# Performance work log

Hardware: AMD Instinct MI355X
Metric: run time of the kernel (lower is better)

The kernel has to match this reference:

```python
import jax, jax.numpy as jnp
import numpy as np
from jax import lax

SCORE_T = 0.05
NMS_T = 0.5
MAXDET = 300


def batch_iou(b1, b2):
    # b1: [K,4], b2: [K,4] -> [K,K]
    lt = jnp.maximum(b1[:, None, :2], b2[None, :, :2])
    rb = jnp.minimum(b1[:, None, 2:], b2[None, :, 2:])
    inter = jnp.clip(rb - lt, 0.0, None).prod(-1)
    a1 = (b1[:, 2:] - b1[:, :2]).prod(-1)
    a2 = (b2[:, 2:] - b2[:, :2]).prod(-1)
    union = a1[:, None] + a2[None, :] - inter
    return inter / jnp.clip(union, 1e-7, None)


def nms_class(boxes, cls_scores):
    # boxes: [N,4], cls_scores: [N]. Mirrors: score>thresh filter, top-k MAXDET
    # candidates, greedy NMS in descending score order.
    s = jnp.where(cls_scores > SCORE_T, cls_scores, -jnp.inf)
    top_s, idx = lax.top_k(s, MAXDET)          # sorted desc, [K]
    b = jnp.take(boxes, idx, axis=0)            # [K,4]
    v = jnp.isfinite(top_s)                     # passed score threshold
    iou = batch_iou(b, b)                       # [K,K]

    def body(kept, i):
        # keep i iff valid and no already-kept box has IoU >= NMS_T with it
        suppressed = jnp.any(jnp.where(kept, iou[i], 0.0) >= NMS_T)
        return kept.at[i].set(v[i] & ~suppressed), None

    kept, _ = lax.scan(body, jnp.zeros(MAXDET, dtype=bool), jnp.arange(MAXDET))
    return top_s, idx, kept


def per_image(boxes, cls):
    # boxes: [N,4], cls: [N,C]
    C = cls.shape[1]
    top_s, idx, kept = jax.vmap(nms_class, in_axes=(None, 1))(boxes, cls)  # [C,K]
    scores_flat = jnp.where(kept, top_s, -jnp.inf).reshape(-1)  # [C*K]
    idx_flat = idx.reshape(-1)
    labels_flat = jnp.repeat(jnp.arange(C), MAXDET)
    fs, fi = lax.top_k(scores_flat, MAXDET)     # global top-k across classes
    valid = jnp.isfinite(fs)
    box_idx = idx_flat[fi]
    out_boxes = jnp.where(valid[:, None], jnp.take(boxes, box_idx, axis=0), -1.0)
    out_scores = jnp.where(valid, fs, -1.0)
    out_labels = jnp.where(valid, labels_flat[fi], -1).astype(jnp.int32)
    return out_boxes, out_scores, out_labels


def setup_inputs() -> dict:
    key = jax.random.key(0)
    k1, k2, k3 = jax.random.split(key, 3)
    B, N, C = 8, 100000, 80
    centers = jax.random.uniform(k1, (B, N, 2), dtype=jnp.float32) * 1024.0
    wh = jax.random.uniform(k2, (B, N, 2), dtype=jnp.float32) * 96.0 + 4.0
    boxes = jnp.concatenate([centers - wh / 2, centers + wh / 2], axis=-1)
    classification = jax.random.uniform(k3, (B, N, C), dtype=jnp.float32)
    return {"boxes": boxes, "classification": classification}


def reference(boxes, classification):
    # Returns (Boxes [B,MAXDET,4], Scores [B,MAXDET], Labels [B,MAXDET] int32),
    # padded with -1 where fewer than MAXDET detections survive.
    return jax.vmap(per_image)(boxes, classification)
```

## Files before the change

### kernel.cpp

```cpp
#include <hip/hip_runtime.h>

#define BIMG 8
#define NBOX 100000
#define NCLS 80
#define KDET 300
#define CAP  2048
#define CAPC 12
#define TPUSH 0.9921875f
#define SCORE_T 0.05f
#define NELEM 8000000
#define NQ    2000000

typedef unsigned long long u64;
typedef unsigned u32;

#define OFF_PUSHCNT 0u
#define ZERO_BYTES  2560u
#define OFF_BUF     4096u
#define OFF_KCNT    (4096u + 10485760u)
#define OFF_KSC     (OFF_KCNT + 2560u)
#define OFF_KIDX    (OFF_KSC + 768000u)

static __device__ __forceinline__ u64 mk_key(float sc, u32 n) {
  return ((u64)__float_as_uint(sc) << 32) | (u32)(~n);
}

static __device__ __forceinline__ u64 shr64(u64 v, int s) {
  return (s >= 64) ? 0ull : (v >> s);
}

static __device__ __forceinline__ void radix_step(const u32* hist, u32* sk,
                                                  u64* spfx, u32* ssel) {
  if (threadIdx.x < 64) {
    const int lane = threadIdx.x;
    const int chunk = 32;
    u32 psum = 0;
    for (int i = 0; i < chunk; ++i) psum += hist[lane * chunk + i];
    u32 suf = psum;
#pragma unroll
    for (int off = 1; off < 64; off <<= 1) {
      u32 o = __shfl_down(suf, off);
      if (lane + off < 64) suf += o;
    }
    u32 k = *sk;
    u64 bal = __ballot(suf >= k);
    if (bal != 0ull) {
      int L = 63 - __clzll((long long)bal);
      if (lane == L) {
        u32 krem = k - (suf - psum);
        int bi = (L + 1) * chunk - 1;
        u32 acc = 0;
        for (;;) {
          acc += hist[bi];
          if (acc >= krem || bi == L * chunk) break;
          --bi;
        }
        *spfx = (*spfx << 11) | (u32)bi;
        *sk = krem - (acc - hist[bi]);
        *ssel = (suf - psum) + acc;
      }
    }
  }
}

static __device__ __forceinline__ void pushone(int c, float sc, u32 n, int b,
                                               u32* lcnt, u64* stage,
                                               u32* pushcnt, u64* buf) {
  u64 key = mk_key(sc, n);
  u32 slot = atomicAdd(&lcnt[c], 1u);
  if (slot < CAPC) {
    stage[c * CAPC + slot] = key;
  } else {
    u32 g = atomicAdd(&pushcnt[b * NCLS + c], 1u);
    if (g < CAP) buf[(size_t)(b * NCLS + c) * CAP + g] = key;
  }
}

__global__ __launch_bounds__(256) void histK(const float* __restrict__ cls,
                                             u32* __restrict__ pushcnt,
                                             u64* __restrict__ buf) {
  __shared__ u32 lcnt[NCLS];
  __shared__ u32 sbase[NCLS];
  __shared__ u64 stage[NCLS * CAPC];

  const int t = threadIdx.x;
  const int b = blockIdx.y;
  for (int i = t; i < NCLS; i += 256) lcnt[i] = 0;
  __syncthreads();

  const float4* base4 = (const float4*)(cls + (size_t)b * NELEM);
  const int start = blockIdx.x * 8192;

#define PROCQ(u) do { \
    float mx = fmaxf(fmaxf(v##u.x, v##u.y), fmaxf(v##u.z, v##u.w)); \
    if (mx >= TPUSH) { \
      const int e0 = q##u * 4; \
      const int c0 = e0 % NCLS; \
      const u32 n = (u32)(e0 / NCLS); \
      if (v##u.x >= TPUSH) pushone(c0 + 0, v##u.x, n, b, lcnt, stage, pushcnt, buf); \
      if (v##u.y >= TPUSH) pushone(c0 + 1, v##u.y, n, b, lcnt, stage, pushcnt, buf); \
      if (v##u.z >= TPUSH) pushone(c0 + 2, v##u.z, n, b, lcnt, stage, pushcnt, buf); \
      if (v##u.w >= TPUSH) pushone(c0 + 3, v##u.w, n, b, lcnt, stage, pushcnt, buf); \
    } } while (0)

  if (start + 8192 <= NQ) {
    for (int it = 0; it < 4; ++it) {
      const int qb = start + it * 2048 + t;
#define LOADF(u) const int q##u = qb + (u) * 256; const float4 v##u = base4[q##u]
      LOADF(0); LOADF(1); LOADF(2); LOADF(3);
      LOADF(4); LOADF(5); LOADF(6); LOADF(7);
#undef LOADF
      PROCQ(0); PROCQ(1); PROCQ(2); PROCQ(3);
      PROCQ(4); PROCQ(5); PROCQ(6); PROCQ(7);
    }
  } else {
    for (int it = 0; it < 4; ++it) {
      const int qb = start + it * 2048 + t;
#define LOADC(u) const int q##u = qb + (u) * 256; \
  const float4 v##u = (q##u < NQ) ? base4[q##u] : make_float4(0.f, 0.f, 0.f, 0.f)
      LOADC(0); LOADC(1); LOADC(2); LOADC(3);
      LOADC(4); LOADC(5); LOADC(6); LOADC(7);
#undef LOADC
      PROCQ(0); PROCQ(1); PROCQ(2); PROCQ(3);
      PROCQ(4); PROCQ(5); PROCQ(6); PROCQ(7);
    }
  }
#undef PROCQ
  __syncthreads();

  if (t < NCLS) {
    u32 cnt = min(lcnt[t], (u32)CAPC);
    sbase[t] = cnt ? atomicAdd(&pushcnt[b * NCLS + t], cnt) : 0u;
  }
  __syncthreads();
  for (int idx = t; idx < NCLS * CAPC; idx += 256) {
    const int c = idx / CAPC;
    const int k = idx - c * CAPC;
    if ((u32)k < min(lcnt[c], (u32)CAPC)) {
      u32 s = sbase[c] + (u32)k;
      if (s < CAP) buf[(size_t)(b * NCLS + c) * CAP + s] = stage[idx];
    }
  }
}

__global__ __launch_bounds__(512) void nmsK(const float* __restrict__ boxes,
                                            const float* __restrict__ cls,
                                            const u32* __restrict__ pushcnt,
                                            u64* __restrict__ buf,
                                            u32* __restrict__ keptCnt,
                                            float* __restrict__ keptScore,
                                            u32* __restrict__ keptIdx) {
  __shared__ float bx[KDET][5];
  __shared__ float scl[KDET];
  __shared__ u32 nn_[KDET];
  __shared__ u64 msk[KDET][5];
  __shared__ u64 tk[512];
  __shared__ u64 keptw[5];
  __shared__ u64 spfx;
  __shared__ u64 sand, sor;
  __shared__ u32 sk, ssel, stcnt;
  __shared__ u32 sfpfx, sfk, sfab, sfeq, sfmode, sfbcnt;

  const int t = threadIdx.x;
  const int bc = blockIdx.x;
  const int b = bc / NCLS;
  u64* bufp = buf + (size_t)bc * CAP;
  u32* hist = (u32*)&msk[0][0];

  if (t == 0) { spfx = 0ull; sk = KDET; stcnt = 0u; sfmode = 0u; sfbcnt = 0u; }

  u32 realcnt = pushcnt[bc];
  const bool dofb = !(realcnt >= (u32)KDET && realcnt <= (u32)CAP);
  if (dofb) {
    const int c = bc % NCLS;
    const float* col = cls + (size_t)b * NELEM + c;
    for (int r = 0; r < 3; ++r) {
      const int shift = (r == 0) ? 21 : (r == 1) ? 10 : 0;
      const int nbins = (r == 2) ? 1024 : 2048;
      for (int i = t; i < nbins; i += 512) hist[i] = 0;
      __syncthreads();
      for (int n = t; n < NBOX; n += 512) {
        float sc = col[(size_t)n * NCLS];
        if (sc > SCORE_T) {
          u32 u = __float_as_uint(sc);
          bool ok = (r == 0) || (r == 1 ? ((u >> 21) == (sfpfx >> 21))
                                        : ((u >> 10) == (sfpfx >> 10)));
          if (ok) atomicAdd(&hist[(u >> shift) & (u32)(nbins - 1)], 1u);
        }
      }
      __syncthreads();
      if (t == 0) {
        if (r == 0) {
          u32 s = 0;
          for (int i = 0; i < nbins; ++i) s += hist[i];
          if (s < KDET) sfmode = 1u;
        }
        if (sfmode == 0u) {
          u32 kk2 = (r == 0) ? (u32)KDET : sfk;
          u32 acc = 0;
          int bi = nbins - 1;
          for (; bi >= 0; --bi) {
            if (acc + hist[bi] >= kk2) break;
            acc += hist[bi];
          }
          sfk = kk2 - acc;
          sfpfx = ((r == 0) ? 0u : sfpfx) | ((u32)bi << shift);
          if (r == 2) { sfeq = hist[bi]; sfab = KDET - sfk; }
        }
      }
      __syncthreads();
      if (sfmode == 1u) break;
    }

    if (sfmode == 1u) {
      for (int n = t; n < NBOX; n += 512) {
        float sc = col[(size_t)n * NCLS];
        if (sc > SCORE_T) {
          u32 g = atomicAdd(&sfbcnt, 1u);
          if (g < CAP) bufp[g] = mk_key(sc, (u32)n);
        }
      }
    } else {
      const u32 ustar = sfpfx;
      const u32 m = sfab, e = sfeq;
      if (m + e <= CAP) {
        for (int n = t; n < NBOX; n += 512) {
          float sc = col[(size_t)n * NCLS];
          if (sc > SCORE_T && __float_as_uint(sc) >= ustar) {
            u32 g = atomicAdd(&sfbcnt, 1u);
            if (g < CAP) bufp[g] = mk_key(sc, (u32)n);
          }
        }
      } else {
        for (int n = t; n < NBOX; n += 512) {
          float sc = col[(size_t)n * NCLS];
          if (sc > SCORE_T && __float_as_uint(sc) > ustar) {
            u32 g = atomicAdd(&sfbcnt, 1u);
            if (g < CAP) bufp[g] = mk_key(sc, (u32)n);
          }
        }
        __syncthreads();
        if (t == 0) {
          u32 room = CAP - m, got = 0;
          for (int n = 0; n < NBOX && got < room; ++n) {
            float sc = col[(size_t)n * NCLS];
            if (sc > SCORE_T && __float_as_uint(sc) == ustar) {
              u32 g = atomicAdd(&sfbcnt, 1u);
              if (g < CAP) bufp[g] = mk_key(sc, (u32)n);
              ++got;
            }
          }
        }
      }
    }
    __threadfence_block();
    __syncthreads();
    realcnt = sfbcnt;
  }
  const int cnt = min((int)realcnt, CAP);

  u64 kk[4];
#pragma unroll
  for (int u = 0; u < 4; ++u) {
    int i = t + u * 512;
    u64 v = 0ull;
    if (i < cnt)
      v = dofb ? *((volatile const u64*)(bufp + i)) : bufp[i];
    kk[u] = v;
  }

  const bool normal = (cnt > KDET);
  int eshift = 0;
  u64 ethr = 1ull;
  if (normal) {
    if (t == 0) { sand = ~0ull; sor = 0ull; }
    __syncthreads();
    {
      u64 ka = ~0ull, ko = 0ull;
#pragma unroll
      for (int u = 0; u < 4; ++u) {
        u64 key = kk[u];
        if (key) { ka &= key; ko |= key; }
      }
#pragma unroll
      for (int off = 32; off > 0; off >>= 1) {
        ka &= __shfl_xor(ka, off);
        ko |= __shfl_xor(ko, off);
      }
      if ((t & 63) == 0) {
        atomicAnd((unsigned long long*)&sand, (unsigned long long)ka);
        atomicOr((unsigned long long*)&sor, (unsigned long long)ko);
      }
    }
    __syncthreads();
    const u64 kand = sand, kor = sor;
    const u64 W = kand ^ kor;
    const int hv = 63 - __clzll((long long)W);
    int s = 11 * (hv / 11);
    if (t == 0) spfx = shr64(kand, s + 11);
    for (;;) {
      for (int i = t; i < 2048; i += 512) hist[i] = 0;
      __syncthreads();
      const u64 pfxHi = spfx;
      const u32 skPrev = sk;
#pragma unroll
      for (int u = 0; u < 4; ++u) {
        u64 key = kk[u];
        if (!key) continue;
        if (shr64(key, s + 11) != pfxHi) continue;
        atomicAdd(&hist[(u32)(key >> s) & 2047u], 1u);
      }
      __syncthreads();
      radix_step(hist, &sk, &spfx, &ssel);
      __syncthreads();
      if ((u32)KDET - skPrev + ssel <= 512u || s == 0) { eshift = s; break; }
      s -= 11;
    }
    ethr = spfx;
  } else {
    __syncthreads();
  }

  tk[t] = 0ull;
  __syncthreads();
  {
    const int lane = t & 63;
    const u64 lmlt = (1ull << lane) - 1ull;
#pragma unroll
    for (int u = 0; u < 4; ++u) {
      u64 key = kk[u];
      bool q = (key != 0ull) && (shr64(key, eshift) >= ethr);
      u64 bal = __ballot(q);
      u32 nw = (u32)__popcll(bal);
      if (nw) {
        u32 base = 0;
        if (lane == 0) base = atomicAdd(&stcnt, nw);
        base = __shfl(base, 0);
        if (q) {
          u32 pos = base + (u32)__popcll(bal & lmlt);
          if (pos < 512) tk[pos] = key;
        }
      }
    }
  }
  __syncthreads();

  const int sc = min((int)stcnt, 512);
  const int M = min(sc, KDET);
  {
    const u64 mykey = tk[t];
    const int scU = (sc + 7) & ~7;
    int rank = 0;
    for (int j = 0; j < scU; j += 8) {
#pragma unroll
      for (int jj = 0; jj < 8; ++jj) rank += (tk[j + jj] > mykey) ? 1 : 0;
    }
    if (mykey != 0ull && rank < KDET) {
      u32 n = ~(u32)mykey;
      scl[rank] = __uint_as_float((u32)(mykey >> 32));
      nn_[rank] = n;
      const float4 bv = *(const float4*)(boxes + ((size_t)b * NBOX + n) * 4);
      bx[rank][0] = bv.x; bx[rank][1] = bv.y; bx[rank][2] = bv.z; bx[rank][3] = bv.w;
    }
  }
  __syncthreads();

  for (int tau = t; tau < KDET * 5; tau += 512) {
    const int i = tau / 5;
    const int w = tau - i * 5;
    u64 m = 0ull;
    const int jb = w << 6;
    if (i < M && jb < i) {
      const int je = min(i, jb + 64);
      const float x1 = bx[i][0], y1 = bx[i][1], x2 = bx[i][2], y2 = bx[i][3];
      const float a1 = (x2 - x1) * (y2 - y1);
      for (int j = jb; j < je; ++j) {
        float lx = fmaxf(x1, bx[j][0]);
        float ly = fmaxf(y1, bx[j][1]);
        float rx = fminf(x2, bx[j][2]);
        float ry = fminf(y2, bx[j][3]);
        float iw = fmaxf(rx - lx, 0.0f), ih = fmaxf(ry - ly, 0.0f);
        float inter = iw * ih;
        float a2 = (bx[j][2] - bx[j][0]) * (bx[j][3] - bx[j][1]);
        float uni = fmaxf(a1 + a2 - inter, 1e-7f);
        float iou = inter / uni;
        if (iou >= 0.5f) m |= 1ull << (j & 63);
      }
    }
    if (i < M) msk[i][w] = m;
  }
  __syncthreads();

  if (t < 64) {
    u64 kwv[5];
#pragma unroll
    for (int w = 0; w < 5; ++w) {
      const int i = w * 64 + t;
      bool pb = (i < M);
      u64 mown = 0ull;
      if (pb) {
#pragma unroll
        for (int w2 = 0; w2 < 5; ++w2)
          if (w2 < w && (msk[i][w2] & kwv[w2])) pb = false;
        mown = msk[i][w];
      }
      u64 kv = 0ull;
      for (;;) {
        u64 bal = __ballot(pb && ((mown & kv) == 0ull));
        if (!bal) break;
        int p = __ffsll((unsigned long long)bal) - 1;
        kv |= 1ull << p;
        if (t == p) pb = false;
      }
      kwv[w] = kv;
      if (t == 0) keptw[w] = kv;
    }
  }
  __syncthreads();

  for (int i = t; i < M; i += 512) {
    if ((keptw[i >> 6] >> (i & 63)) & 1ull) {
      int rank = 0;
      for (int w = 0; w < (i >> 6); ++w) rank += __popcll(keptw[w]);
      rank += __popcll(keptw[i >> 6] & ((1ull << (i & 63)) - 1ull));
      keptScore[(size_t)bc * KDET + rank] = scl[i];
      keptIdx[(size_t)bc * KDET + rank] = nn_[i];
    }
  }
  if (t == 0) {
    int tot = 0;
    for (int w = 0; w < 5; ++w) tot += __popcll(keptw[w]);
    keptCnt[bc] = (u32)tot;
  }
}

__global__ __launch_bounds__(512) void mergeK(const float* __restrict__ boxes,
                                              const u32* __restrict__ keptCnt,
                                              const float* __restrict__ keptScore,
                                              const u32* __restrict__ keptIdx,
                                              float* __restrict__ out) {
  __shared__ u32 hist[2048];
  __shared__ int msc[NCLS];
  __shared__ u64 tk[512];
  __shared__ u64 spfx, sand, sor;
  __shared__ u32 sk, ssel, stcnt, smtot;

  const int t = threadIdx.x;
  const int b = blockIdx.x;
  if (t < NCLS) msc[t] = min((int)keptCnt[b * NCLS + t], KDET);
  if (t == 0) {
    spfx = 0ull; sk = KDET; stcnt = 0u; smtot = 0u; sand = ~0ull; sor = 0ull;
  }
  __syncthreads();

  const float* ksc = keptScore + (size_t)b * NCLS * KDET;
#define MKEY(idx, key) do { \
    int c_ = (idx) / KDET, r_ = (idx) - c_ * KDET; \
    key = (r_ < msc[c_]) ? ((u64)__float_as_uint(ksc[idx]) << 32) | (u32)(~(u32)(idx)) \
                         : 0ull; \
  } while (0)

  {
    u64 ka = ~0ull, ko = 0ull;
    u32 mycnt = 0;
    for (int idx = t; idx < NCLS * KDET; idx += 512) {
      u64 key; MKEY(idx, key);
      if (key) { ka &= key; ko |= key; ++mycnt; }
    }
#pragma unroll
    for (int off = 32; off > 0; off >>= 1) {
      ka &= __shfl_xor(ka, off);
      ko |= __shfl_xor(ko, off);
      mycnt += __shfl_xor(mycnt, off);
    }
    if ((t & 63) == 0) {
      atomicAnd((unsigned long long*)&sand, (unsigned long long)ka);
      atomicOr((unsigned long long*)&sor, (unsigned long long)ko);
      atomicAdd(&smtot, mycnt);
    }
  }
  __syncthreads();

  const bool mnormal = ((int)smtot > KDET);
  int eshift = 0;
  u64 ethr = 1ull;
  if (mnormal) {
    const u64 kand = sand, kor = sor;
    const u64 W = kand ^ kor;
    const int hv = 63 - __clzll((long long)W);
    int s = 11 * (hv / 11);
    if (t == 0) spfx = shr64(kand, s + 11);
    for (;;) {
      for (int i = t; i < 2048; i += 512) hist[i] = 0;
      __syncthreads();
      const u64 pfxHi = spfx;
      const u32 skPrev = sk;
      for (int idx = t; idx < NCLS * KDET; idx += 512) {
        u64 key; MKEY(idx, key);
        if (!key) continue;
        if (shr64(key, s + 11) != pfxHi) continue;
        atomicAdd(&hist[(u32)(key >> s) & 2047u], 1u);
      }
      __syncthreads();
      radix_step(hist, &sk, &spfx, &ssel);
      __syncthreads();
      if ((u32)KDET - skPrev + ssel <= 512u || s == 0) { eshift = s; break; }
      s -= 11;
    }
    ethr = spfx;
  }

  tk[t] = 0ull;
  __syncthreads();
  {
    const int lane = t & 63;
    const u64 lmlt = (1ull << lane) - 1ull;
    for (int i0 = 0; i0 < NCLS * KDET; i0 += 512) {
      const int idx = i0 + t;
      u64 key = 0ull;
      if (idx < NCLS * KDET) MKEY(idx, key);
      bool q = (key != 0ull) && (shr64(key, eshift) >= ethr);
      u64 bal = __ballot(q);
      u32 nw = (u32)__popcll(bal);
      if (nw) {
        u32 base = 0;
        if (lane == 0) base = atomicAdd(&stcnt, nw);
        base = __shfl(base, 0);
        if (q) {
          u32 pos = base + (u32)__popcll(bal & lmlt);
          if (pos < 512) tk[pos] = key;
        }
      }
    }
  }
  __syncthreads();
#undef MKEY

  const int sc = min((int)stcnt, 512);
  {
    const u64 mykey = tk[t];
    const int scU = (sc + 7) & ~7;
    int rank = 0;
    for (int j = 0; j < scU; j += 8) {
#pragma unroll
      for (int jj = 0; jj < 8; ++jj) rank += (tk[j + jj] > mykey) ? 1 : 0;
    }
    __syncthreads();
    tk[t] = 0ull;
    __syncthreads();
    if (mykey != 0ull && rank < KDET) tk[rank] = mykey;
  }
  __syncthreads();

  if (t < KDET) {
    float* ob = out + ((size_t)b * KDET + t) * 4;
    float* os = out + (size_t)BIMG * KDET * 4;
    float* ol = os + (size_t)BIMG * KDET;
    u64 key = tk[t];
    if (key == 0ull) {
      *(float4*)ob = make_float4(-1.f, -1.f, -1.f, -1.f);
      os[(size_t)b * KDET + t] = -1.f;
      ol[(size_t)b * KDET + t] = -1.f;
    } else {
      u32 fi = ~(u32)key;
      int c = fi / KDET, r = fi - c * KDET;
      u32 n = keptIdx[((size_t)b * NCLS + c) * KDET + r];
      *(float4*)ob = *(const float4*)(boxes + ((size_t)b * NBOX + n) * 4);
      os[(size_t)b * KDET + t] = __uint_as_float((u32)(key >> 32));
      ol[(size_t)b * KDET + t] = (float)c;
    }
  }
}

extern "C" void kernel_launch(void* const* d_in, const int* in_sizes, int n_in,
                              void* d_out, int out_size, void* d_ws, size_t ws_size,
                              hipStream_t stream) {
  const float* boxes = (const float*)d_in[0];
  const float* cls = (const float*)d_in[1];
  float* out = (float*)d_out;
  char* ws = (char*)d_ws;

  u32* pushcnt = (u32*)(ws + OFF_PUSHCNT);
  u64* buf = (u64*)(ws + OFF_BUF);
  u32* keptCnt = (u32*)(ws + OFF_KCNT);
  float* keptScore = (float*)(ws + OFF_KSC);
  u32* keptIdx = (u32*)(ws + OFF_KIDX);

  (void)hipMemsetAsync(ws + OFF_PUSHCNT, 0, ZERO_BYTES, stream);

  histK<<<dim3(245, BIMG), 256, 0, stream>>>(cls, pushcnt, buf);
  nmsK<<<BIMG * NCLS, 512, 0, stream>>>(boxes, cls, pushcnt, buf, keptCnt,
                                        keptScore, keptIdx);
  mergeK<<<BIMG, 512, 0, stream>>>(boxes, keptCnt, keptScore, keptIdx, out);
}
```

Baseline: 520.3 us.

## Replace per-class NMS and merge with per-image score-ordered chunked greedy NMS

The candidate push threshold is raised, and all candidates for an image go into one global buffer through a single per-image atomic counter. This replaces the per-class staged buffers. The separate per-class NMS kernel (640 blocks) and the merge kernel become one 1024-thread block per image. That block takes candidates in descending global score order in chunks of 512, runs class-aware greedy NMS against the boxes already kept, and stops once 300 are kept. A slow per-class radix-select fallback over the full score matrix runs when the buffer overflows or too few detections survive. The aim is to cut push atomics, buffer traffic and the redundant per-class work, at the cost of only 8 blocks of parallelism in the NMS stage.

```diff
diff --git a/kernel.cpp b/kernel.cpp
--- a/kernel.cpp
+++ b/kernel.cpp
@@ -4,9 +4,10 @@
 #define NBOX 100000
 #define NCLS 80
 #define KDET 300
-#define CAP  2048
-#define CAPC 12
-#define TPUSH 0.9921875f
+#define CAP2 8192
+#define PCCAP 2048
+#define BUFSTRIDE (NCLS * PCCAP)
+#define TPUSH2 0.999755859375f
 #define SCORE_T 0.05f
 #define NELEM 8000000
 #define NQ    2000000
@@ -14,19 +15,15 @@
 typedef unsigned long long u64;
 typedef unsigned u32;
 
-#define OFF_PUSHCNT 0u
-#define ZERO_BYTES  2560u
-#define OFF_BUF     4096u
-#define OFF_KCNT    (4096u + 10485760u)
-#define OFF_KSC     (OFF_KCNT + 2560u)
-#define OFF_KIDX    (OFF_KSC + 768000u)
-
-static __device__ __forceinline__ u64 mk_key(float sc, u32 n) {
-  return ((u64)__float_as_uint(sc) << 32) | (u32)(~n);
-}
+#define OFF_PCNT 0u
+#define ZERO_BYTES 32u
+#define OFF_BUF  4096u
 
 static __device__ __forceinline__ u64 shr64(u64 v, int s) {
   return (s >= 64) ? 0ull : (v >> s);
+}
+static __device__ __forceinline__ u64 key2(float sc, u32 c, u32 n) {
+  return ((u64)__float_as_uint(sc) << 32) | (u32)(~(c * (u32)NBOX + n));
 }
 
 static __device__ __forceinline__ void radix_step(const u32* hist, u32* sk,
@@ -63,44 +60,28 @@
   }
 }
 
-static __device__ __forceinline__ void pushone(int c, float sc, u32 n, int b,
-                                               u32* lcnt, u64* stage,
-                                               u32* pushcnt, u64* buf) {
-  u64 key = mk_key(sc, n);
-  u32 slot = atomicAdd(&lcnt[c], 1u);
-  if (slot < CAPC) {
-    stage[c * CAPC + slot] = key;
-  } else {
-    u32 g = atomicAdd(&pushcnt[b * NCLS + c], 1u);
-    if (g < CAP) buf[(size_t)(b * NCLS + c) * CAP + g] = key;
-  }
-}
-
 __global__ __launch_bounds__(256) void histK(const float* __restrict__ cls,
-                                             u32* __restrict__ pushcnt,
+                                             u32* __restrict__ pcnt,
                                              u64* __restrict__ buf) {
-  __shared__ u32 lcnt[NCLS];
-  __shared__ u32 sbase[NCLS];
-  __shared__ u64 stage[NCLS * CAPC];
-
   const int t = threadIdx.x;
   const int b = blockIdx.y;
-  for (int i = t; i < NCLS; i += 256) lcnt[i] = 0;
-  __syncthreads();
-
   const float4* base4 = (const float4*)(cls + (size_t)b * NELEM);
+  u64* bufb = buf + (size_t)b * BUFSTRIDE;
   const int start = blockIdx.x * 8192;
 
+#define PUSH1(cc, sc_) do { \
+    u32 g = atomicAdd(&pcnt[b], 1u); \
+    if (g < CAP2) bufb[g] = key2(sc_, (u32)(cc), (u32)n); } while (0)
 #define PROCQ(u) do { \
     float mx = fmaxf(fmaxf(v##u.x, v##u.y), fmaxf(v##u.z, v##u.w)); \
-    if (mx >= TPUSH) { \
+    if (mx >= TPUSH2) { \
       const int e0 = q##u * 4; \
       const int c0 = e0 % NCLS; \
-      const u32 n = (u32)(e0 / NCLS); \
-      if (v##u.x >= TPUSH) pushone(c0 + 0, v##u.x, n, b, lcnt, stage, pushcnt, buf); \
-      if (v##u.y >= TPUSH) pushone(c0 + 1, v##u.y, n, b, lcnt, stage, pushcnt, buf); \
-      if (v##u.z >= TPUSH) pushone(c0 + 2, v##u.z, n, b, lcnt, stage, pushcnt, buf); \
-      if (v##u.w >= TPUSH) pushone(c0 + 3, v##u.w, n, b, lcnt, stage, pushcnt, buf); \
+      const int n = e0 / NCLS; \
+      if (v##u.x >= TPUSH2) PUSH1(c0 + 0, v##u.x); \
+      if (v##u.y >= TPUSH2) PUSH1(c0 + 1, v##u.y); \
+      if (v##u.z >= TPUSH2) PUSH1(c0 + 2, v##u.z); \
+      if (v##u.w >= TPUSH2) PUSH1(c0 + 3, v##u.w); \
     } } while (0)
 
   if (start + 8192 <= NQ) {
@@ -126,448 +107,371 @@
     }
   }
 #undef PROCQ
-  __syncthreads();
-
-  if (t < NCLS) {
-    u32 cnt = min(lcnt[t], (u32)CAPC);
-    sbase[t] = cnt ? atomicAdd(&pushcnt[b * NCLS + t], cnt) : 0u;
-  }
-  __syncthreads();
-  for (int idx = t; idx < NCLS * CAPC; idx += 256) {
-    const int c = idx / CAPC;
-    const int k = idx - c * CAPC;
-    if ((u32)k < min(lcnt[c], (u32)CAPC)) {
-      u32 s = sbase[c] + (u32)k;
-      if (s < CAP) buf[(size_t)(b * NCLS + c) * CAP + s] = stage[idx];
-    }
-  }
-}
-
-__global__ __launch_bounds__(512) void nmsK(const float* __restrict__ boxes,
-                                            const float* __restrict__ cls,
-                                            const u32* __restrict__ pushcnt,
-                                            u64* __restrict__ buf,
-                                            u32* __restrict__ keptCnt,
-                                            float* __restrict__ keptScore,
-                                            u32* __restrict__ keptIdx) {
-  __shared__ float bx[KDET][5];
-  __shared__ float scl[KDET];
-  __shared__ u32 nn_[KDET];
-  __shared__ u64 msk[KDET][5];
-  __shared__ u64 tk[512];
-  __shared__ u64 keptw[5];
-  __shared__ u64 spfx;
-  __shared__ u64 sand, sor;
-  __shared__ u32 sk, ssel, stcnt;
-  __shared__ u32 sfpfx, sfk, sfab, sfeq, sfmode, sfbcnt;
-
-  const int t = threadIdx.x;
-  const int bc = blockIdx.x;
-  const int b = bc / NCLS;
-  u64* bufp = buf + (size_t)bc * CAP;
+#undef PUSH1
+}
+
+__global__ __launch_bounds__(1024) void nmsK(const float* __restrict__ boxes,
+                                             const float* __restrict__ cls,
+                                             const u32* __restrict__ pcnt,
+                                             u64* __restrict__ buf,
+                                             float* __restrict__ out) {
+  __shared__ u64 msk[512][8];
+  __shared__ u64 ks[512];
+  __shared__ float bx[512][5];
+  __shared__ u32 ci[512];
+  __shared__ u32 valid[512];
+  __shared__ u64 kkey[KDET];
+  __shared__ float kbx[KDET][4];
+  __shared__ u32 ccnt[NCLS], chunkcls[NCLS];
+  __shared__ u64 keptw[8];
+  __shared__ u64 sand, sor, spfx, swin;
+  __shared__ u32 sk, ssel, stcnt, srem, skcnt, scap;
+  __shared__ u32 srtot, sfpfx, sfk, sfab, sfeq, sfmode, slocal;
+
   u32* hist = (u32*)&msk[0][0];
-
-  if (t == 0) { spfx = 0ull; sk = KDET; stcnt = 0u; sfmode = 0u; sfbcnt = 0u; }
-
-  u32 realcnt = pushcnt[bc];
-  const bool dofb = !(realcnt >= (u32)KDET && realcnt <= (u32)CAP);
-  if (dofb) {
-    const int c = bc % NCLS;
-    const float* col = cls + (size_t)b * NELEM + c;
-    for (int r = 0; r < 3; ++r) {
-      const int shift = (r == 0) ? 21 : (r == 1) ? 10 : 0;
-      const int nbins = (r == 2) ? 1024 : 2048;
-      for (int i = t; i < nbins; i += 512) hist[i] = 0;
-      __syncthreads();
-      for (int n = t; n < NBOX; n += 512) {
-        float sc = col[(size_t)n * NCLS];
-        if (sc > SCORE_T) {
-          u32 u = __float_as_uint(sc);
-          bool ok = (r == 0) || (r == 1 ? ((u >> 21) == (sfpfx >> 21))
-                                        : ((u >> 10) == (sfpfx >> 10)));
-          if (ok) atomicAdd(&hist[(u >> shift) & (u32)(nbins - 1)], 1u);
-        }
-      }
-      __syncthreads();
-      if (t == 0) {
-        if (r == 0) {
-          u32 s = 0;
-          for (int i = 0; i < nbins; ++i) s += hist[i];
-          if (s < KDET) sfmode = 1u;
-        }
-        if (sfmode == 0u) {
-          u32 kk2 = (r == 0) ? (u32)KDET : sfk;
-          u32 acc = 0;
-          int bi = nbins - 1;
-          for (; bi >= 0; --bi) {
-            if (acc + hist[bi] >= kk2) break;
-            acc += hist[bi];
-          }
-          sfk = kk2 - acc;
-          sfpfx = ((r == 0) ? 0u : sfpfx) | ((u32)bi << shift);
-          if (r == 2) { sfeq = hist[bi]; sfab = KDET - sfk; }
-        }
-      }
-      __syncthreads();
-      if (sfmode == 1u) break;
-    }
-
-    if (sfmode == 1u) {
-      for (int n = t; n < NBOX; n += 512) {
-        float sc = col[(size_t)n * NCLS];
-        if (sc > SCORE_T) {
-          u32 g = atomicAdd(&sfbcnt, 1u);
-          if (g < CAP) bufp[g] = mk_key(sc, (u32)n);
-        }
-      }
-    } else {
-      const u32 ustar = sfpfx;
-      const u32 m = sfab, e = sfeq;
-      if (m + e <= CAP) {
-        for (int n = t; n < NBOX; n += 512) {
-          float sc = col[(size_t)n * NCLS];
-          if (sc > SCORE_T && __float_as_uint(sc) >= ustar) {
-            u32 g = atomicAdd(&sfbcnt, 1u);
-            if (g < CAP) bufp[g] = mk_key(sc, (u32)n);
-          }
-        }
-      } else {
-        for (int n = t; n < NBOX; n += 512) {
-          float sc = col[(size_t)n * NCLS];
-          if (sc > SCORE_T && __float_as_uint(sc) > ustar) {
-            u32 g = atomicAdd(&sfbcnt, 1u);
-            if (g < CAP) bufp[g] = mk_key(sc, (u32)n);
-          }
-        }
-        __syncthreads();
-        if (t == 0) {
-          u32 room = CAP - m, got = 0;
-          for (int n = 0; n < NBOX && got < room; ++n) {
-            float sc = col[(size_t)n * NCLS];
-            if (sc > SCORE_T && __float_as_uint(sc) == ustar) {
-              u32 g = atomicAdd(&sfbcnt, 1u);
-              if (g < CAP) bufp[g] = mk_key(sc, (u32)n);
-              ++got;
-            }
-          }
-        }
-      }
-    }
-    __threadfence_block();
-    __syncthreads();
-    realcnt = sfbcnt;
-  }
-  const int cnt = min((int)realcnt, CAP);
-
-  u64 kk[4];
-#pragma unroll
-  for (int u = 0; u < 4; ++u) {
-    int i = t + u * 512;
-    u64 v = 0ull;
-    if (i < cnt)
-      v = dofb ? *((volatile const u64*)(bufp + i)) : bufp[i];
-    kk[u] = v;
-  }
-
-  const bool normal = (cnt > KDET);
-  int eshift = 0;
-  u64 ethr = 1ull;
-  if (normal) {
-    if (t == 0) { sand = ~0ull; sor = 0ull; }
-    __syncthreads();
-    {
-      u64 ka = ~0ull, ko = 0ull;
-#pragma unroll
-      for (int u = 0; u < 4; ++u) {
-        u64 key = kk[u];
-        if (key) { ka &= key; ko |= key; }
-      }
-#pragma unroll
-      for (int off = 32; off > 0; off >>= 1) {
-        ka &= __shfl_xor(ka, off);
-        ko |= __shfl_xor(ko, off);
-      }
-      if ((t & 63) == 0) {
-        atomicAnd((unsigned long long*)&sand, (unsigned long long)ka);
-        atomicOr((unsigned long long*)&sor, (unsigned long long)ko);
-      }
-    }
-    __syncthreads();
-    const u64 kand = sand, kor = sor;
-    const u64 W = kand ^ kor;
-    const int hv = 63 - __clzll((long long)W);
-    int s = 11 * (hv / 11);
-    if (t == 0) spfx = shr64(kand, s + 11);
-    for (;;) {
-      for (int i = t; i < 2048; i += 512) hist[i] = 0;
-      __syncthreads();
-      const u64 pfxHi = spfx;
-      const u32 skPrev = sk;
-#pragma unroll
-      for (int u = 0; u < 4; ++u) {
-        u64 key = kk[u];
-        if (!key) continue;
-        if (shr64(key, s + 11) != pfxHi) continue;
-        atomicAdd(&hist[(u32)(key >> s) & 2047u], 1u);
-      }
-      __syncthreads();
-      radix_step(hist, &sk, &spfx, &ssel);
-      __syncthreads();
-      if ((u32)KDET - skPrev + ssel <= 512u || s == 0) { eshift = s; break; }
-      s -= 11;
-    }
-    ethr = spfx;
-  } else {
-    __syncthreads();
-  }
-
-  tk[t] = 0ull;
-  __syncthreads();
-  {
-    const int lane = t & 63;
-    const u64 lmlt = (1ull << lane) - 1ull;
-#pragma unroll
-    for (int u = 0; u < 4; ++u) {
-      u64 key = kk[u];
-      bool q = (key != 0ull) && (shr64(key, eshift) >= ethr);
-      u64 bal = __ballot(q);
-      u32 nw = (u32)__popcll(bal);
-      if (nw) {
-        u32 base = 0;
-        if (lane == 0) base = atomicAdd(&stcnt, nw);
-        base = __shfl(base, 0);
-        if (q) {
-          u32 pos = base + (u32)__popcll(bal & lmlt);
-          if (pos < 512) tk[pos] = key;
-        }
-      }
-    }
-  }
-  __syncthreads();
-
-  const int sc = min((int)stcnt, 512);
-  const int M = min(sc, KDET);
-  {
-    const u64 mykey = tk[t];
-    const int scU = (sc + 7) & ~7;
-    int rank = 0;
-    for (int j = 0; j < scU; j += 8) {
-#pragma unroll
-      for (int jj = 0; jj < 8; ++jj) rank += (tk[j + jj] > mykey) ? 1 : 0;
-    }
-    if (mykey != 0ull && rank < KDET) {
-      u32 n = ~(u32)mykey;
-      scl[rank] = __uint_as_float((u32)(mykey >> 32));
-      nn_[rank] = n;
-      const float4 bv = *(const float4*)(boxes + ((size_t)b * NBOX + n) * 4);
-      bx[rank][0] = bv.x; bx[rank][1] = bv.y; bx[rank][2] = bv.z; bx[rank][3] = bv.w;
-    }
-  }
-  __syncthreads();
-
-  for (int tau = t; tau < KDET * 5; tau += 512) {
-    const int i = tau / 5;
-    const int w = tau - i * 5;
-    u64 m = 0ull;
-    const int jb = w << 6;
-    if (i < M && jb < i) {
-      const int je = min(i, jb + 64);
-      const float x1 = bx[i][0], y1 = bx[i][1], x2 = bx[i][2], y2 = bx[i][3];
-      const float a1 = (x2 - x1) * (y2 - y1);
-      for (int j = jb; j < je; ++j) {
-        float lx = fmaxf(x1, bx[j][0]);
-        float ly = fmaxf(y1, bx[j][1]);
-        float rx = fminf(x2, bx[j][2]);
-        float ry = fminf(y2, bx[j][3]);
-        float iw = fmaxf(rx - lx, 0.0f), ih = fmaxf(ry - ly, 0.0f);
-        float inter = iw * ih;
-        float a2 = (bx[j][2] - bx[j][0]) * (bx[j][3] - bx[j][1]);
-        float uni = fmaxf(a1 + a2 - inter, 1e-7f);
-        float iou = inter / uni;
-        if (iou >= 0.5f) m |= 1ull << (j & 63);
-      }
-    }
-    if (i < M) msk[i][w] = m;
-  }
-  __syncthreads();
-
-  if (t < 64) {
-    u64 kwv[5];
-#pragma unroll
-    for (int w = 0; w < 5; ++w) {
-      const int i = w * 64 + t;
-      bool pb = (i < M);
-      u64 mown = 0ull;
-      if (pb) {
-#pragma unroll
-        for (int w2 = 0; w2 < 5; ++w2)
-          if (w2 < w && (msk[i][w2] & kwv[w2])) pb = false;
-        mown = msk[i][w];
-      }
-      u64 kv = 0ull;
-      for (;;) {
-        u64 bal = __ballot(pb && ((mown & kv) == 0ull));
-        if (!bal) break;
-        int p = __ffsll((unsigned long long)bal) - 1;
-        kv |= 1ull << p;
-        if (t == p) pb = false;
-      }
-      kwv[w] = kv;
-      if (t == 0) keptw[w] = kv;
-    }
-  }
-  __syncthreads();
-
-  for (int i = t; i < M; i += 512) {
-    if ((keptw[i >> 6] >> (i & 63)) & 1ull) {
-      int rank = 0;
-      for (int w = 0; w < (i >> 6); ++w) rank += __popcll(keptw[w]);
-      rank += __popcll(keptw[i >> 6] & ((1ull << (i & 63)) - 1ull));
-      keptScore[(size_t)bc * KDET + rank] = scl[i];
-      keptIdx[(size_t)bc * KDET + rank] = nn_[i];
-    }
-  }
-  if (t == 0) {
-    int tot = 0;
-    for (int w = 0; w < 5; ++w) tot += __popcll(keptw[w]);
-    keptCnt[bc] = (u32)tot;
-  }
-}
-
-__global__ __launch_bounds__(512) void mergeK(const float* __restrict__ boxes,
-                                              const u32* __restrict__ keptCnt,
-                                              const float* __restrict__ keptScore,
-                                              const u32* __restrict__ keptIdx,
-                                              float* __restrict__ out) {
-  __shared__ u32 hist[2048];
-  __shared__ int msc[NCLS];
-  __shared__ u64 tk[512];
-  __shared__ u64 spfx, sand, sor;
-  __shared__ u32 sk, ssel, stcnt, smtot;
-
+  u64* tkbuf = (u64*)&msk[0][0] + 1024;
   const int t = threadIdx.x;
   const int b = blockIdx.x;
-  if (t < NCLS) msc[t] = min((int)keptCnt[b * NCLS + t], KDET);
-  if (t == 0) {
-    spfx = 0ull; sk = KDET; stcnt = 0u; smtot = 0u; sand = ~0ull; sor = 0ull;
+  volatile u64* bufb = (volatile u64*)(buf + (size_t)b * BUFSTRIDE);
+
+  u32 cnt = pcnt[b];
+  bool rare = (cnt > CAP2);
+
+  for (;;) {
+    if (rare) {
+      if (t == 0) srtot = 0;
+      __syncthreads();
+      for (int c = 0; c < NCLS; ++c) {
+        const float* col = cls + (size_t)b * NELEM + c;
+        if (t == 0) { sfmode = 0u; slocal = 0u; }
+        for (int r = 0; r < 3; ++r) {
+          const int shift = (r == 0) ? 21 : (r == 1) ? 10 : 0;
+          const int nb = (r == 2) ? 1024 : 2048;
+          for (int i = t; i < nb; i += 1024) hist[i] = 0;
+          __syncthreads();
+          for (int n = t; n < NBOX; n += 1024) {
+            float s2 = col[(size_t)n * NCLS];
+            if (s2 > SCORE_T) {
+              u32 u = __float_as_uint(s2);
+              bool ok = (r == 0) || (r == 1 ? ((u >> 21) == (sfpfx >> 21))
+                                            : ((u >> 10) == (sfpfx >> 10)));
+              if (ok) atomicAdd(&hist[(u >> shift) & (u32)(nb - 1)], 1u);
+            }
+          }
+          __syncthreads();
+          if (t == 0) {
+            if (r == 0) {
+              u32 s = 0;
+              for (int i = 0; i < nb; ++i) s += hist[i];
+              if (s < KDET) sfmode = 1u;
+            }
+            if (sfmode == 0u) {
+              u32 kk2 = (r == 0) ? (u32)KDET : sfk;
+              u32 acc = 0;
+              int bi = nb - 1;
+              for (; bi >= 0; --bi) {
+                if (acc + hist[bi] >= kk2) break;
+                acc += hist[bi];
+              }
+              sfk = kk2 - acc;
+              sfpfx = ((r == 0) ? 0u : sfpfx) | ((u32)bi << shift);
+              if (r == 2) { sfeq = hist[bi]; sfab = KDET - sfk; }
+            }
+          }
+          __syncthreads();
+          if (sfmode == 1u) break;
+        }
+        const u32 base = srtot;
+        if (sfmode == 1u) {
+          for (int n = t; n < NBOX; n += 1024) {
+            float s2 = col[(size_t)n * NCLS];
+            if (s2 > SCORE_T) {
+              u32 g = atomicAdd(&slocal, 1u);
+              if (g < PCCAP) bufb[base + g] = key2(s2, (u32)c, (u32)n);
+            }
+          }
+        } else {
+          const u32 ustar = sfpfx;
+          const u32 m = sfab, e = sfeq;
+          if (m + e <= PCCAP) {
+            for (int n = t; n < NBOX; n += 1024) {
+              float s2 = col[(size_t)n * NCLS];
+              if (s2 > SCORE_T && __float_as_uint(s2) >= ustar) {
+                u32 g = atomicAdd(&slocal, 1u);
+                if (g < PCCAP) bufb[base + g] = key2(s2, (u32)c, (u32)n);
+              }
+            }
+          } else {
+            for (int n = t; n < NBOX; n += 1024) {
+              float s2 = col[(size_t)n * NCLS];
+              if (s2 > SCORE_T && __float_as_uint(s2) > ustar) {
+                u32 g = atomicAdd(&slocal, 1u);
+                if (g < PCCAP) bufb[base + g] = key2(s2, (u32)c, (u32)n);
+              }
+            }
+            __syncthreads();
+            if (t == 0) {
+              u32 room = PCCAP - slocal, got = 0;
+              for (int n = 0; n < NBOX && got < room; ++n) {
+                float s2 = col[(size_t)n * NCLS];
+                if (s2 > SCORE_T && __float_as_uint(s2) == ustar) {
+                  u32 g = atomicAdd(&slocal, 1u);
+                  if (g < PCCAP) bufb[base + g] = key2(s2, (u32)c, (u32)n);
+                  ++got;
+                }
+              }
+            }
+          }
+        }
+        __syncthreads();
+        if (t == 0) srtot = base + min(slocal, (u32)PCCAP);
+        __syncthreads();
+      }
+      __threadfence_block();
+      __syncthreads();
+      cnt = srtot;
+    }
+
+    if (t == 0) { skcnt = 0u; swin = ~0ull; }
+    for (int i = t; i < NCLS; i += 1024) ccnt[i] = 0u;
+    __syncthreads();
+
+    for (;;) {
+      if (t == 0) { sand = ~0ull; sor = 0ull; srem = 0u; stcnt = 0u; scap = 0u; }
+      if (t < 512) tkbuf[t] = 0ull;
+      for (int i = t; i < NCLS; i += 1024) chunkcls[i] = 0u;
+      __syncthreads();
+      {
+        const u64 win = swin;
+        u64 ka = ~0ull, ko = 0ull;
+        u32 rc = 0;
+        for (u32 idx = t; idx < cnt; idx += 1024) {
+          u64 key = bufb[idx];
+          if (key < win) { ka &= key; ko |= key; ++rc; }
+        }
+#pragma unroll
+        for (int off = 32; off > 0; off >>= 1) {
+          ka &= __shfl_xor(ka, off);
+          ko |= __shfl_xor(ko, off);
+          rc += __shfl_xor(rc, off);
+        }
+        if ((t & 63) == 0) {
+          atomicAnd((unsigned long long*)&sand, (unsigned long long)ka);
+          atomicOr((unsigned long long*)&sor, (unsigned long long)ko);
+          atomicAdd(&srem, rc);
+        }
+      }
+      __syncthreads();
+      if (srem == 0u) break;
+      const u64 win = swin;
+      const u32 G = min(512u, srem);
+      int eshift = 0;
+      u64 ethr = 1ull;
+      const bool allsel = (srem <= 512u);
+      if (!allsel) {
+        const u64 kand = sand, kor = sor;
+        const u64 W = kand ^ kor;
+        const int hv = 63 - __clzll((long long)W);
+        int s = 11 * (hv / 11);
+        if (t == 0) { spfx = shr64(kand, s + 11); sk = G; }
+        __syncthreads();
+        for (;;) {
+          for (int i = t; i < 2048; i += 1024) hist[i] = 0u;
+          __syncthreads();
+          const u64 pfxHi = spfx;
+          const u32 skPrev = sk;
+          for (u32 idx = t; idx < cnt; idx += 1024) {
+            u64 key = bufb[idx];
+            if (key < win && shr64(key, s + 11) == pfxHi)
+              atomicAdd(&hist[(u32)(key >> s) & 2047u], 1u);
+          }
+          __syncthreads();
+          radix_step(hist, &sk, &spfx, &ssel);
+          __syncthreads();
+          if (G - skPrev + ssel <= 512u || s == 0) { eshift = s; break; }
+          s -= 11;
+        }
+        ethr = spfx;
+      }
+      {
+        const int lane = t & 63;
+        const u64 lml = (1ull << lane) - 1ull;
+        for (u32 i0 = 0; i0 < cnt; i0 += 1024) {
+          const u32 idx = i0 + t;
+          u64 key = (idx < cnt) ? bufb[idx] : 0ull;
+          bool q = (key != 0ull) && (key < win) &&
+                   (allsel || shr64(key, eshift) >= ethr);
+          u64 bal = __ballot(q);
+          u32 nw = (u32)__popcll(bal);
+          if (nw) {
+            u32 base = 0;
+            if (lane == 0) base = atomicAdd(&stcnt, nw);
+            base = __shfl(base, 0);
+            if (q) {
+              u32 pos = base + (u32)__popcll(bal & lml);
+              if (pos < 512u) tkbuf[pos] = key;
+            }
+          }
+        }
+      }
+      __syncthreads();
+      const int S = min((int)stcnt, 512);
+
+      if (t < 512) {
+        const u64 mykey = tkbuf[t];
+        const int SU = (S + 7) & ~7;
+        int rank = 0;
+        for (int j = 0; j < SU; j += 8) {
+#pragma unroll
+          for (int jj = 0; jj < 8; ++jj) rank += (tkbuf[j + jj] > mykey) ? 1 : 0;
+        }
+        if (mykey != 0ull) {
+          ks[rank] = mykey;
+          u32 e2 = ~(u32)mykey;
+          u32 c = e2 / (u32)NBOX;
+          u32 n = e2 - c * (u32)NBOX;
+          ci[rank] = c;
+          const float4 bv = *(const float4*)(boxes + ((size_t)b * NBOX + n) * 4);
+          bx[rank][0] = bv.x; bx[rank][1] = bv.y;
+          bx[rank][2] = bv.z; bx[rank][3] = bv.w;
+        }
+        if (t >= S) { ks[t] = 0ull; }
+        valid[t] = (t < S) ? 1u : 0u;
+      }
+      __syncthreads();
+      if (t < S) atomicAdd(&chunkcls[ci[t]], 1u);
+      __syncthreads();
+      if (t < NCLS && (ccnt[t] + chunkcls[t] > (u32)KDET)) atomicOr(&scap, 1u);
+      __syncthreads();
+      if (scap) {
+        if (t < S) {
+          u32 c = ci[t], r = ccnt[c];
+          for (int j = 0; j < t; ++j) r += (ci[j] == c) ? 1u : 0u;
+          if (r >= (u32)KDET) valid[t] = 0u;
+        }
+        __syncthreads();
+      }
+      const int kc0 = (int)skcnt;
+      if (kc0 > 0) {
+        if (t < S && valid[t]) {
+          const float x1 = bx[t][0], y1 = bx[t][1], x2 = bx[t][2], y2 = bx[t][3];
+          const float a1 = (x2 - x1) * (y2 - y1);
+          const u32 c = ci[t];
+          const int ke = min(kc0, KDET);
+          for (int k = 0; k < ke; ++k) {
+            u32 kcls = (~(u32)kkey[k]) / (u32)NBOX;
+            if (kcls != c) continue;
+            float lx = fmaxf(x1, kbx[k][0]);
+            float ly = fmaxf(y1, kbx[k][1]);
+            float rx = fminf(x2, kbx[k][2]);
+            float ry = fminf(y2, kbx[k][3]);
+            float iw = fmaxf(rx - lx, 0.0f), ih = fmaxf(ry - ly, 0.0f);
+            float inter = iw * ih;
+            float a2 = (kbx[k][2] - kbx[k][0]) * (kbx[k][3] - kbx[k][1]);
+            float uni = fmaxf(a1 + a2 - inter, 1e-7f);
+            float iou = inter / uni;
+            if (iou >= 0.5f) { valid[t] = 0u; break; }
+          }
+        }
+        __syncthreads();
+      }
+      for (int tau = t; tau < 512 * 8; tau += 1024) {
+        const int i = tau >> 3;
+        const int w = tau & 7;
+        u64 m = 0ull;
+        const int jb = w << 6;
+        if (i < S && valid[i] && jb < i) {
+          const int je = min(i, jb + 64);
+          const float x1 = bx[i][0], y1 = bx[i][1], x2 = bx[i][2], y2 = bx[i][3];
+          const float a1 = (x2 - x1) * (y2 - y1);
+          const u32 c = ci[i];
+          for (int j = jb; j < je; ++j) {
+            if (ci[j] != c) continue;
+            float lx = fmaxf(x1, bx[j][0]);
+            float ly = fmaxf(y1, bx[j][1]);
+            float rx = fminf(x2, bx[j][2]);
+            float ry = fminf(y2, bx[j][3]);
+            float iw = fmaxf(rx - lx, 0.0f), ih = fmaxf(ry - ly, 0.0f);
+            float inter = iw * ih;
+            float a2 = (bx[j][2] - bx[j][0]) * (bx[j][3] - bx[j][1]);
+            float uni = fmaxf(a1 + a2 - inter, 1e-7f);
+            float iou = inter / uni;
+            if (iou >= 0.5f) m |= 1ull << (j & 63);
+          }
+        }
+        msk[i][w] = m;
+      }
+      __syncthreads();
+      if (t < 64) {
+        u64 kwv[8];
+#pragma unroll
+        for (int w = 0; w < 8; ++w) {
+          const int i = w * 64 + t;
+          bool pb = (i < S) && valid[i];
+          u64 mown = 0ull;
+          if (pb) {
+#pragma unroll
+            for (int w2 = 0; w2 < 8; ++w2)
+              if (w2 < w && (msk[i][w2] & kwv[w2])) pb = false;
+            mown = msk[i][w];
+          }
+          u64 kv = 0ull;
+          for (;;) {
+            u64 bal = __ballot(pb && ((mown & kv) == 0ull));
+            if (!bal) break;
+            int p = __ffsll((unsigned long long)bal) - 1;
+            kv |= 1ull << p;
+            if (t == p) pb = false;
+          }
+          kwv[w] = kv;
+          if (t == 0) keptw[w] = kv;
+        }
+      }
+      __syncthreads();
+      if (t < S) {
+        if ((keptw[t >> 6] >> (t & 63)) & 1ull) {
+          int g = kc0;
+          for (int w = 0; w < (t >> 6); ++w) g += __popcll(keptw[w]);
+          g += __popcll(keptw[t >> 6] & ((1ull << (t & 63)) - 1ull));
+          if (g < KDET) {
+            kkey[g] = ks[t];
+            kbx[g][0] = bx[t][0]; kbx[g][1] = bx[t][1];
+            kbx[g][2] = bx[t][2]; kbx[g][3] = bx[t][3];
+          }
+        }
+      }
+      if (t == 0) {
+        int tot = 0;
+        for (int w = 0; w < 8; ++w) tot += __popcll(keptw[w]);
+        skcnt = (u32)(kc0 + tot);
+        swin = ks[S - 1];
+      }
+      if (t < NCLS) ccnt[t] += chunkcls[t];
+      __syncthreads();
+      if (skcnt >= (u32)KDET) break;
+    }
+
+    if (skcnt >= (u32)KDET || rare) break;
+    rare = true;
   }
+
   __syncthreads();
-
-  const float* ksc = keptScore + (size_t)b * NCLS * KDET;
-#define MKEY(idx, key) do { \
-    int c_ = (idx) / KDET, r_ = (idx) - c_ * KDET; \
-    key = (r_ < msc[c_]) ? ((u64)__float_as_uint(ksc[idx]) << 32) | (u32)(~(u32)(idx)) \
-                         : 0ull; \
-  } while (0)
-
-  {
-    u64 ka = ~0ull, ko = 0ull;
-    u32 mycnt = 0;
-    for (int idx = t; idx < NCLS * KDET; idx += 512) {
-      u64 key; MKEY(idx, key);
-      if (key) { ka &= key; ko |= key; ++mycnt; }
-    }
-#pragma unroll
-    for (int off = 32; off > 0; off >>= 1) {
-      ka &= __shfl_xor(ka, off);
-      ko |= __shfl_xor(ko, off);
-      mycnt += __shfl_xor(mycnt, off);
-    }
-    if ((t & 63) == 0) {
-      atomicAnd((unsigned long long*)&sand, (unsigned long long)ka);
-      atomicOr((unsigned long long*)&sor, (unsigned long long)ko);
-      atomicAdd(&smtot, mycnt);
-    }
-  }
-  __syncthreads();
-
-  const bool mnormal = ((int)smtot > KDET);
-  int eshift = 0;
-  u64 ethr = 1ull;
-  if (mnormal) {
-    const u64 kand = sand, kor = sor;
-    const u64 W = kand ^ kor;
-    const int hv = 63 - __clzll((long long)W);
-    int s = 11 * (hv / 11);
-    if (t == 0) spfx = shr64(kand, s + 11);
-    for (;;) {
-      for (int i = t; i < 2048; i += 512) hist[i] = 0;
-      __syncthreads();
-      const u64 pfxHi = spfx;
-      const u32 skPrev = sk;
-      for (int idx = t; idx < NCLS * KDET; idx += 512) {
-        u64 key; MKEY(idx, key);
-        if (!key) continue;
-        if (shr64(key, s + 11) != pfxHi) continue;
-        atomicAdd(&hist[(u32)(key >> s) & 2047u], 1u);
-      }
-      __syncthreads();
-      radix_step(hist, &sk, &spfx, &ssel);
-      __syncthreads();
-      if ((u32)KDET - skPrev + ssel <= 512u || s == 0) { eshift = s; break; }
-      s -= 11;
-    }
-    ethr = spfx;
-  }
-
-  tk[t] = 0ull;
-  __syncthreads();
-  {
-    const int lane = t & 63;
-    const u64 lmlt = (1ull << lane) - 1ull;
-    for (int i0 = 0; i0 < NCLS * KDET; i0 += 512) {
-      const int idx = i0 + t;
-      u64 key = 0ull;
-      if (idx < NCLS * KDET) MKEY(idx, key);
-      bool q = (key != 0ull) && (shr64(key, eshift) >= ethr);
-      u64 bal = __ballot(q);
-      u32 nw = (u32)__popcll(bal);
-      if (nw) {
-        u32 base = 0;
-        if (lane == 0) base = atomicAdd(&stcnt, nw);
-        base = __shfl(base, 0);
-        if (q) {
-          u32 pos = base + (u32)__popcll(bal & lmlt);
-          if (pos < 512) tk[pos] = key;
-        }
-      }
-    }
-  }
-  __syncthreads();
-#undef MKEY
-
-  const int sc = min((int)stcnt, 512);
-  {
-    const u64 mykey = tk[t];
-    const int scU = (sc + 7) & ~7;
-    int rank = 0;
-    for (int j = 0; j < scU; j += 8) {
-#pragma unroll
-      for (int jj = 0; jj < 8; ++jj) rank += (tk[j + jj] > mykey) ? 1 : 0;
-    }
-    __syncthreads();
-    tk[t] = 0ull;
-    __syncthreads();
-    if (mykey != 0ull && rank < KDET) tk[rank] = mykey;
-  }
-  __syncthreads();
-
+  const int kc = min((int)skcnt, KDET);
   if (t < KDET) {
     float* ob = out + ((size_t)b * KDET + t) * 4;
     float* os = out + (size_t)BIMG * KDET * 4;
     float* ol = os + (size_t)BIMG * KDET;
-    u64 key = tk[t];
-    if (key == 0ull) {
+    if (t < kc) {
+      u64 key = kkey[t];
+      u32 e2 = ~(u32)key;
+      u32 c = e2 / (u32)NBOX;
+      *(float4*)ob = make_float4(kbx[t][0], kbx[t][1], kbx[t][2], kbx[t][3]);
+      os[(size_t)b * KDET + t] = __uint_as_float((u32)(key >> 32));
+      ol[(size_t)b * KDET + t] = (float)c;
+    } else {
       *(float4*)ob = make_float4(-1.f, -1.f, -1.f, -1.f);
       os[(size_t)b * KDET + t] = -1.f;
       ol[(size_t)b * KDET + t] = -1.f;
-    } else {
-      u32 fi = ~(u32)key;
-      int c = fi / KDET, r = fi - c * KDET;
-      u32 n = keptIdx[((size_t)b * NCLS + c) * KDET + r];
-      *(float4*)ob = *(const float4*)(boxes + ((size_t)b * NBOX + n) * 4);
-      os[(size_t)b * KDET + t] = __uint_as_float((u32)(key >> 32));
-      ol[(size_t)b * KDET + t] = (float)c;
     }
   }
 }
@@ -580,16 +484,11 @@
   float* out = (float*)d_out;
   char* ws = (char*)d_ws;
 
-  u32* pushcnt = (u32*)(ws + OFF_PUSHCNT);
+  u32* pcnt = (u32*)(ws + OFF_PCNT);
   u64* buf = (u64*)(ws + OFF_BUF);
-  u32* keptCnt = (u32*)(ws + OFF_KCNT);
-  float* keptScore = (float*)(ws + OFF_KSC);
-  u32* keptIdx = (u32*)(ws + OFF_KIDX);
-
-  (void)hipMemsetAsync(ws + OFF_PUSHCNT, 0, ZERO_BYTES, stream);
-
-  histK<<<dim3(245, BIMG), 256, 0, stream>>>(cls, pushcnt, buf);
-  nmsK<<<BIMG * NCLS, 512, 0, stream>>>(boxes, cls, pushcnt, buf, keptCnt,
-                                        keptScore, keptIdx);
-  mergeK<<<BIMG, 512, 0, stream>>>(boxes, keptCnt, keptScore, keptIdx, out);
-}
+
+  (void)hipMemsetAsync(ws + OFF_PCNT, 0, ZERO_BYTES, stream);
+
+  histK<<<dim3(245, BIMG), 256, 0, stream>>>(cls, pcnt, buf);
+  nmsK<<<BIMG, 1024, 0, stream>>>(boxes, cls, pcnt, buf, out);
+}
```

New measurement: 540.2 us. 3.8% more time.
